# Kernel tuning notes

Hardware: AMD Instinct MI355X
Metric: run time of the kernel (lower is better)

The kernel has to match this reference:

```python
import jax, jax.numpy as jnp
import numpy as np

B, N, L, D, DI = 128, 64, 33, 512, 768  # batch, num_images, cooccurrence_num+1, CLIP dim, inst dim


def setup_inputs() -> dict:
    key = jax.random.key(0)
    ks = jax.random.split(key, 8)
    return {
        "image_features": jax.random.normal(ks[0], (B, N, D), jnp.float32),
        "image_mask": jax.random.randint(ks[1], (B, N), 0, 2).astype(jnp.int32),
        "landmark_feature": jax.random.normal(ks[2], (B, L, D), jnp.float32),
        "inst": jax.random.normal(ks[3], (B, DI), jnp.float32),
        # scoring_module = Linear(512+768 -> 512) -> ReLU -> LayerNorm(512) -> Dropout(eval: identity)
        "W_score": jax.random.normal(ks[4], (DI + D, D), jnp.float32) * 0.02,
        "b_score": jnp.zeros((D,), jnp.float32),
        "ln_gamma": jnp.ones((D,), jnp.float32),
        "ln_beta": jnp.zeros((D,), jnp.float32),
    }


def _l2norm(x):
    return x / jnp.linalg.norm(x, axis=-1, keepdims=True)


def reference(image_features, image_mask, landmark_feature, inst,
              W_score, b_score, ln_gamma, ln_beta):
    LN_EPS = 1e-12
    mask = image_mask == 1  # [B, N]

    img = _l2norm(image_features)          # [B, N, D]
    lmk = _l2norm(landmark_feature)        # [B, L, D]
    img = jnp.where(mask[:, :, None], img, 0.0)
    img_mean = img.mean(axis=1)            # [B, D]

    # scoring_module on cat([inst, img_mean]) -> ReLU -> LayerNorm (Dropout is identity in eval)
    h = jnp.concatenate([inst, img_mean], axis=-1) @ W_score + b_score  # [B, D]
    h = jax.nn.relu(h)
    mu = h.mean(axis=-1, keepdims=True)
    var = h.var(axis=-1, keepdims=True)    # biased, as in torch LayerNorm
    h = (h - mu) / jnp.sqrt(var + LN_EPS) * ln_gamma + ln_beta
    inst_feat = _l2norm(h)                 # [B, D]

    cooccurrence_weight = 100.0 * jnp.einsum('bd,bld->bl', inst_feat, lmk)  # [B, L]
    candidate_prob = 100.0 * jnp.einsum('bnd,bld->bnl', img, lmk)           # [B, N, L]
    candidate_prob = jnp.where(mask[:, :, None], candidate_prob, -jnp.inf)
    p = jax.nn.softmax(candidate_prob, axis=1)                              # softmax over images

    corrected_landmark_feature = jnp.einsum('bnl,bl,bld->bnd', p, cooccurrence_weight, lmk)  # [B, N, D]
    corrected_candidate_prob = jnp.einsum('bnl,bl->bn', p, cooccurrence_weight)              # [B, N]
    corrected_candidate_prob = jnp.where(mask, corrected_candidate_prob, -jnp.inf)
    return corrected_landmark_feature, corrected_candidate_prob
```

## Files before the change

kernel.cpp:

```cpp
#include <hip/hip_runtime.h>
#include <math.h>

#define BB 128
#define NN 64
#define LL 33
#define DD 512
#define DIN 768

#define NEG_BIG (-3.0e38f)

typedef __attribute__((ext_vector_type(8))) short bf16x8;
typedef __attribute__((ext_vector_type(4))) float f32x4;

#define WS_ASW   0
#define WS_BSW   (WS_ASW + BB*3*16*64*4)
#define WS_LMK16 (WS_BSW + BB*4*16*64*4)
#define WS_MEANP (WS_LMK16 + BB*LL*DD/2)
#define WS_PART  (WS_MEANP + BB*16*DD)
#define WS_INSTF (WS_PART + BB*8*DD)
#define WS_S     (WS_INSTF + BB*DD)

__device__ __forceinline__ float wave_sum(float v) {
#pragma unroll
  for (int m = 32; m; m >>= 1) v += __shfl_xor(v, m);
  return v;
}
__device__ __forceinline__ float wave_max(float v) {
#pragma unroll
  for (int m = 32; m; m >>= 1) v = fmaxf(v, __shfl_xor(v, m));
  return v;
}
__device__ __forceinline__ unsigned f2bf(float f) {
  unsigned u = __float_as_uint(f);
  return (u + 0x7FFFu + ((u >> 16) & 1u)) >> 16;
}
__device__ __forceinline__ unsigned pk2(float a, float b) {
  return f2bf(a) | (f2bf(b) << 16);
}
__device__ __forceinline__ float bflo(unsigned u) { return __uint_as_float(u << 16); }
__device__ __forceinline__ float bfhi(unsigned u) { return __uint_as_float(u & 0xFFFF0000u); }

__global__ __launch_bounds__(256) void k_prep_v15(
    const float* __restrict__ img_in, const int* __restrict__ mask,
    const float* __restrict__ lmk_in, unsigned int* __restrict__ AswW,
    unsigned int* __restrict__ BswW, unsigned short* __restrict__ lmk16,
    float* __restrict__ meanp) {
  uint4* Asw = (uint4*)AswW;
  uint4* Bsw = (uint4*)BswW;
  int o = blockIdx.x;
  int blk = (o & 7) * 64 + (o >> 3);
  int b = blk >> 2, q = blk & 3;
  int t = threadIdx.x;
  int w = t >> 6, lane = t & 63;

  int nbase = q * 16 + w * 4;
  const float4* ib = (const float4*)(img_in + ((size_t)b * NN + nbase) * DD);
  float4 r[4][2];
#pragma unroll
  for (int i = 0; i < 4; i++) {
    r[i][0] = ib[i * 128 + lane * 2];
    r[i][1] = ib[i * 128 + lane * 2 + 1];
  }
  const int* mb = mask + b * NN + nbase;
  float macc[8];
#pragma unroll
  for (int j = 0; j < 8; j++) macc[j] = 0.f;
#pragma unroll
  for (int i = 0; i < 4; i++) {
    float4 v0 = r[i][0], v1 = r[i][1];
    float ss = v0.x * v0.x + v0.y * v0.y + v0.z * v0.z + v0.w * v0.w +
               v1.x * v1.x + v1.y * v1.y + v1.z * v1.z + v1.w * v1.w;
    ss = wave_sum(ss);
    float keep = (mb[i] == 1) ? 1.f : 0.f;
    float s = keep / sqrtf(ss);
    v0.x *= s; v0.y *= s; v0.z *= s; v0.w *= s;
    v1.x *= s; v1.y *= s; v1.z *= s; v1.w *= s;
    macc[0] += v0.x; macc[1] += v0.y; macc[2] += v0.z; macc[3] += v0.w;
    macc[4] += v1.x; macc[5] += v1.y; macc[6] += v1.z; macc[7] += v1.w;
    int rg = nbase + i;
    uint4 p = make_uint4(pk2(v0.x, v0.y), pk2(v0.z, v0.w), pk2(v1.x, v1.y),
                         pk2(v1.z, v1.w));
    Bsw[(((size_t)b * 4 + (rg >> 4)) * 16 + (lane >> 2)) * 64 + (rg & 15) +
        16 * (lane & 3)] = p;
  }
  {
    float* mp = meanp + ((size_t)b * 16 + q * 4 + w) * DD + lane * 8;
    float4 m0 = {macc[0], macc[1], macc[2], macc[3]};
    float4 m1 = {macc[4], macc[5], macc[6], macc[7]};
    *(float4*)mp = m0;
    *(float4*)(mp + 4) = m1;
  }

  int lr = q * 8 + w * 2;
  bool xtra = (q == 0) && (w == 3);
  if (xtra) {
#pragma unroll
    for (int kk = 0; kk < 16; kk++)
      if (lane & 15)
        Asw[(((size_t)b * 3 + 2) * 16 + kk) * 64 + lane] = make_uint4(0, 0, 0, 0);
  }
#pragma unroll
  for (int k = 0; k < 3; k++) {
    int row = (k < 2) ? (lr + k) : 32;
    if (k == 2 && !xtra) break;
    const float4* lb = (const float4*)(lmk_in + ((size_t)b * LL + row) * DD);
    float4 v0 = lb[lane * 2], v1 = lb[lane * 2 + 1];
    float ss = v0.x * v0.x + v0.y * v0.y + v0.z * v0.z + v0.w * v0.w +
               v1.x * v1.x + v1.y * v1.y + v1.z * v1.z + v1.w * v1.w;
    ss = wave_sum(ss);
    float s = 1.f / sqrtf(ss);
    v0.x *= s; v0.y *= s; v0.z *= s; v0.w *= s;
    v1.x *= s; v1.y *= s; v1.z *= s; v1.w *= s;
    uint4 p = make_uint4(pk2(v0.x, v0.y), pk2(v0.z, v0.w), pk2(v1.x, v1.y),
                         pk2(v1.z, v1.w));
    ((uint4*)lmk16)[((size_t)b * LL + row) * 64 + lane] = p;
    Asw[(((size_t)b * 3 + (row >> 4)) * 16 + (lane >> 2)) * 64 + (row & 15) +
        16 * (lane & 3)] = p;
  }
}

#define KCH 160
__global__ void k_gemm_part_v15(const float* __restrict__ inst,
                                const float* __restrict__ meanp,
                                const float* __restrict__ W,
                                float* __restrict__ part) {
  int o = blockIdx.x;
  int blk = (o & 7) * 32 + (o >> 3);
  __shared__ float xs[KCH][4];
  int bg = blk >> 3;
  int c = blk & 7;
  int b0 = bg * 4;
  int t = threadIdx.x;
  int k0 = c * KCH;
  for (int i = t; i < KCH * 4; i += 256) {
    int kk = i >> 2;
    int j = i & 3;
    int kg = k0 + kk;
    float val;
    if (kg < DIN) {
      val = inst[(size_t)(b0 + j) * DIN + kg];
    } else {
      const float* mp = meanp + (size_t)(b0 + j) * 16 * DD + (kg - DIN);
      float s = 0.f;
#pragma unroll
      for (int p = 0; p < 16; p++) s += mp[p * DD];
      val = s * (1.f / 64.f);
    }
    xs[kk][j] = val;
  }
  __syncthreads();
  const float2* Wp = (const float2*)(W + (size_t)k0 * DD);
  float2 a0 = {0.f, 0.f}, a1 = {0.f, 0.f}, a2 = {0.f, 0.f}, a3 = {0.f, 0.f};
#pragma unroll 4
  for (int kk = 0; kk < KCH; kk++) {
    float2 w = Wp[kk * 256 + t];
    float4 xv = *(const float4*)&xs[kk][0];
    a0.x += xv.x * w.x; a0.y += xv.x * w.y;
    a1.x += xv.y * w.x; a1.y += xv.y * w.y;
    a2.x += xv.z * w.x; a2.y += xv.z * w.y;
    a3.x += xv.w * w.x; a3.y += xv.w * w.y;
  }
  float2* pp = (float2*)part;
  pp[(((size_t)(b0 + 0) * 8 + c) * DD >> 1) + t] = a0;
  pp[(((size_t)(b0 + 1) * 8 + c) * DD >> 1) + t] = a1;
  pp[(((size_t)(b0 + 2) * 8 + c) * DD >> 1) + t] = a2;
  pp[(((size_t)(b0 + 3) * 8 + c) * DD >> 1) + t] = a3;
}

__device__ __forceinline__ float blk_sum2(float v, float* red4, int t) {
  v = wave_sum(v);
  __syncthreads();
  if ((t & 63) == 0) red4[t >> 6] = v;
  __syncthreads();
  return red4[0] + red4[1] + red4[2] + red4[3];
}

__global__ __launch_bounds__(256) void k_ssm_v15(
    const unsigned int* __restrict__ AswW, const unsigned int* __restrict__ BswW,
    const float* __restrict__ part, const float* __restrict__ bias,
    const float* __restrict__ gamma, const float* __restrict__ beta,
    const unsigned short* __restrict__ lmk16, const int* __restrict__ mask,
    float* __restrict__ q) {
  __shared__ float st[16][68];
  __shared__ float fi[DD];
  __shared__ float red4[4];
  const bf16x8* Asw = (const bf16x8*)AswW;
  const bf16x8* Bsw = (const bf16x8*)BswW;
  int o = blockIdx.x;
  int blk = (o & 7) * 48 + (o >> 3);
  int b = blk / 3, mt = blk - b * 3;
  int t = threadIdx.x;
  int nt = t >> 6, lane = t & 63;

  {
    const float* pb = part + (size_t)b * 8 * DD;
    float sa = 0.f, sb = 0.f;
#pragma unroll
    for (int c = 0; c < 8; c++) {
      sa += pb[c * DD + t];
      sb += pb[c * DD + t + 256];
    }
    float rva = fmaxf(sa + bias[t], 0.f);
    float rvb = fmaxf(sb + bias[t + 256], 0.f);
    float s1 = blk_sum2(rva + rvb, red4, t);
    float s2 = blk_sum2(rva * rva + rvb * rvb, red4, t);
    float mu = s1 * (1.f / DD);
    float var = s2 * (1.f / DD) - mu * mu;
    float inv = 1.f / sqrtf(var + 1e-12f);
    float ya = (rva - mu) * inv * gamma[t] + beta[t];
    float yb = (rvb - mu) * inv * gamma[t + 256] + beta[t + 256];
    float n2 = blk_sum2(ya * ya + yb * yb, red4, t);
    float rn = 1.f / sqrtf(n2);
    fi[t] = ya * rn;
    fi[t + 256] = yb * rn;
  }

  {
    const bf16x8* ap = Asw + ((size_t)(b * 3 + mt) * 16) * 64 + lane;
    const bf16x8* bp = Bsw + ((size_t)(b * 4 + nt) * 16) * 64 + lane;
    f32x4 acc = {0.f, 0.f, 0.f, 0.f};
#pragma unroll
    for (int kk = 0; kk < 16; kk++)
      acc = __builtin_amdgcn_mfma_f32_16x16x32_bf16(ap[kk * 64], bp[kk * 64],
                                                    acc, 0, 0, 0);
    int col = nt * 16 + (lane & 15);
    int rbase = (lane >> 4) << 2;
#pragma unroll
    for (int reg = 0; reg < 4; reg++) st[rbase + reg][col] = 100.f * acc[reg];
  }
  __syncthreads();

  bool keep = (mask[b * NN + lane] == 1);
  const float4* fi4 = (const float4*)fi;
  float4 f0 = fi4[lane * 2], f1 = fi4[lane * 2 + 1];
#pragma unroll
  for (int j = 0; j < 4; j++) {
    int lrow = nt * 4 + j;
    int l = mt * 16 + lrow;
    if (l >= LL) break;
    float s = st[lrow][lane];
    uint4 u = ((const uint4*)(lmk16 + ((size_t)b * LL + l) * DD))[lane];
    float dp = f0.x * bflo(u.x) + f0.y * bfhi(u.x) + f0.z * bflo(u.y) +
               f0.w * bfhi(u.y) + f1.x * bflo(u.z) + f1.y * bfhi(u.z) +
               f1.z * bflo(u.w) + f1.w * bfhi(u.w);
    dp = wave_sum(dp);
    float cw = 100.f * dp;
    float v = keep ? s : NEG_BIG;
    float mx = wave_max(v);
    float e = keep ? __expf(s - mx) : 0.f;
    float Z = wave_sum(e);
    float sc = (Z > 0.f) ? (cw / Z) : 0.f;
    q[((size_t)b * LL + l) * NN + lane] = e * sc;
  }
}

__global__ void k_out_v15(const float* __restrict__ S,
                          const unsigned short* __restrict__ lmk16,
                          const int* __restrict__ mask,
                          float* __restrict__ out1,
                          float* __restrict__ out2) {
  __shared__ __align__(16) float qs[LL][8];
  int o = blockIdx.x;
  int blk = (o & 7) * 128 + (o >> 3);
  int b = blk >> 3;
  int nt = blk & 7;
  int t = threadIdx.x;
  for (int i = t; i < 8 * LL; i += 256) {
    int l = i >> 3;
    int n_loc = i & 7;
    qs[l][n_loc] = S[((size_t)b * LL + l) * NN + nt * 8 + n_loc];
  }
  __syncthreads();
  if (t < 8) {
    float ssum = 0.f;
#pragma unroll
    for (int l = 0; l < LL; l++) ssum += qs[l][t];
    int n = nt * 8 + t;
    out2[b * NN + n] = (mask[b * NN + n] == 1) ? ssum : NEG_BIG;
  }
  int d0 = t * 2;
  float accx[8], accy[8];
#pragma unroll
  for (int n = 0; n < 8; n++) { accx[n] = 0.f; accy[n] = 0.f; }
  const unsigned short* lmkb = lmk16 + (size_t)b * LL * DD;
#pragma unroll 4
  for (int l = 0; l < LL; l++) {
    unsigned u = *(const unsigned*)(lmkb + (size_t)l * DD + d0);
    float lvx = bflo(u), lvy = bfhi(u);
    float4 q0 = *(const float4*)&qs[l][0];
    float4 q1 = *(const float4*)&qs[l][4];
    accx[0] += q0.x * lvx; accy[0] += q0.x * lvy;
    accx[1] += q0.y * lvx; accy[1] += q0.y * lvy;
    accx[2] += q0.z * lvx; accy[2] += q0.z * lvy;
    accx[3] += q0.w * lvx; accy[3] += q0.w * lvy;
    accx[4] += q1.x * lvx; accy[4] += q1.x * lvy;
    accx[5] += q1.y * lvx; accy[5] += q1.y * lvy;
    accx[6] += q1.z * lvx; accy[6] += q1.z * lvy;
    accx[7] += q1.w * lvx; accy[7] += q1.w * lvy;
  }
#pragma unroll
  for (int n = 0; n < 8; n++) {
    float2 oo = {accx[n], accy[n]};
    *(float2*)&out1[(((size_t)b * NN) + nt * 8 + n) * DD + d0] = oo;
  }
}

extern "C" void kernel_launch(void* const* d_in, const int* in_sizes, int n_in,
                              void* d_out, int out_size, void* d_ws, size_t ws_size,
                              hipStream_t stream) {
  const float* image_features = (const float*)d_in[0];
  const int* image_mask = (const int*)d_in[1];
  const float* landmark = (const float*)d_in[2];
  const float* inst = (const float*)d_in[3];
  const float* W = (const float*)d_in[4];
  const float* bias = (const float*)d_in[5];
  const float* gamma = (const float*)d_in[6];
  const float* beta = (const float*)d_in[7];

  float* ws = (float*)d_ws;
  unsigned int* Asw = (unsigned int*)(ws + WS_ASW);
  unsigned int* Bsw = (unsigned int*)(ws + WS_BSW);
  unsigned short* lmk16 = (unsigned short*)(ws + WS_LMK16);
  float* ws_meanp = ws + WS_MEANP;
  float* ws_part = ws + WS_PART;
  float* ws_S = ws + WS_S;

  float* out1 = (float*)d_out;
  float* out2 = (float*)d_out + (size_t)BB * NN * DD;

  k_prep_v15<<<BB * 4, 256, 0, stream>>>(image_features, image_mask, landmark,
                                         Asw, Bsw, lmk16, ws_meanp);
  k_gemm_part_v15<<<(BB / 4) * 8, 256, 0, stream>>>(inst, ws_meanp, W, ws_part);
  k_ssm_v15<<<BB * 3, 256, 0, stream>>>((const unsigned int*)Asw,
                                        (const unsigned int*)Bsw, ws_part, bias,
                                        gamma, beta, lmk16, image_mask, ws_S);
  k_out_v15<<<BB * 8, 256, 0, stream>>>(ws_S, lmk16, image_mask, out1, out2);
}
```

Measured before the change: 48.96 us.

## Overlap inst-part GEMM with prep kernel and pre-reduce image mean in-block

Splits the scoring GEMM into two parts. The inst half (K=768) runs as extra blocks inside the prep kernel, so it overlaps with the normalization work. The image-mean half runs in a small follow-up kernel. The prep blocks now reduce their four waves' partial means through shared memory before writing, which cuts the meanp partials from 16 to 4 per batch. This lowers the work left on the critical path after prep, at the cost of a heterogeneous prep launch and 16 partials per batch to sum in the ssm kernel.

```diff
diff --git a/kernel.cpp b/kernel.cpp
--- a/kernel.cpp
+++ b/kernel.cpp
@@ -16,9 +16,8 @@
 #define WS_BSW   (WS_ASW + BB*3*16*64*4)
 #define WS_LMK16 (WS_BSW + BB*4*16*64*4)
 #define WS_MEANP (WS_LMK16 + BB*LL*DD/2)
-#define WS_PART  (WS_MEANP + BB*16*DD)
-#define WS_INSTF (WS_PART + BB*8*DD)
-#define WS_S     (WS_INSTF + BB*DD)
+#define WS_PART  (WS_MEANP + BB*4*DD)
+#define WS_S     (WS_PART + BB*16*DD)
 
 __device__ __forceinline__ float wave_sum(float v) {
 #pragma unroll
@@ -40,119 +39,148 @@
 __device__ __forceinline__ float bflo(unsigned u) { return __uint_as_float(u << 16); }
 __device__ __forceinline__ float bfhi(unsigned u) { return __uint_as_float(u & 0xFFFF0000u); }
 
-__global__ __launch_bounds__(256) void k_prep_v15(
+__global__ __launch_bounds__(256) void k_prep_v16(
     const float* __restrict__ img_in, const int* __restrict__ mask,
-    const float* __restrict__ lmk_in, unsigned int* __restrict__ AswW,
+    const float* __restrict__ lmk_in, const float* __restrict__ inst,
+    const float* __restrict__ W, unsigned int* __restrict__ AswW,
     unsigned int* __restrict__ BswW, unsigned short* __restrict__ lmk16,
-    float* __restrict__ meanp) {
-  uint4* Asw = (uint4*)AswW;
-  uint4* Bsw = (uint4*)BswW;
+    float* __restrict__ meanp, float* __restrict__ part) {
+  __shared__ __align__(16) float shbuf[2048];
+  int t = threadIdx.x;
+
+  if (blockIdx.x < 512) {
+    uint4* Asw = (uint4*)AswW;
+    uint4* Bsw = (uint4*)BswW;
+    int o = blockIdx.x;
+    int blk = (o & 7) * 64 + (o >> 3);
+    int b = blk >> 2, q = blk & 3;
+    int w = t >> 6, lane = t & 63;
+
+    int nbase = q * 16 + w * 4;
+    const float4* ib = (const float4*)(img_in + ((size_t)b * NN + nbase) * DD);
+    float4 r[4][2];
+#pragma unroll
+    for (int i = 0; i < 4; i++) {
+      r[i][0] = ib[i * 128 + lane * 2];
+      r[i][1] = ib[i * 128 + lane * 2 + 1];
+    }
+    const int* mb = mask + b * NN + nbase;
+    float macc[8];
+#pragma unroll
+    for (int j = 0; j < 8; j++) macc[j] = 0.f;
+#pragma unroll
+    for (int i = 0; i < 4; i++) {
+      float4 v0 = r[i][0], v1 = r[i][1];
+      float ss = v0.x * v0.x + v0.y * v0.y + v0.z * v0.z + v0.w * v0.w +
+                 v1.x * v1.x + v1.y * v1.y + v1.z * v1.z + v1.w * v1.w;
+      ss = wave_sum(ss);
+      float keep = (mb[i] == 1) ? 1.f : 0.f;
+      float s = keep / sqrtf(ss);
+      v0.x *= s; v0.y *= s; v0.z *= s; v0.w *= s;
+      v1.x *= s; v1.y *= s; v1.z *= s; v1.w *= s;
+      macc[0] += v0.x; macc[1] += v0.y; macc[2] += v0.z; macc[3] += v0.w;
+      macc[4] += v1.x; macc[5] += v1.y; macc[6] += v1.z; macc[7] += v1.w;
+      int rg = nbase + i;
+      uint4 p = make_uint4(pk2(v0.x, v0.y), pk2(v0.z, v0.w), pk2(v1.x, v1.y),
+                           pk2(v1.z, v1.w));
+      Bsw[(((size_t)b * 4 + (rg >> 4)) * 16 + (lane >> 2)) * 64 + (rg & 15) +
+          16 * (lane & 3)] = p;
+    }
+    {
+      float4 m0 = {macc[0], macc[1], macc[2], macc[3]};
+      float4 m1 = {macc[4], macc[5], macc[6], macc[7]};
+      *(float4*)&shbuf[w * 512 + lane * 8] = m0;
+      *(float4*)&shbuf[w * 512 + lane * 8 + 4] = m1;
+    }
+    __syncthreads();
+    {
+      float s0 = shbuf[t] + shbuf[512 + t] + shbuf[1024 + t] + shbuf[1536 + t];
+      float s1 = shbuf[t + 256] + shbuf[512 + t + 256] + shbuf[1024 + t + 256] +
+                 shbuf[1536 + t + 256];
+      meanp[((size_t)b * 4 + q) * DD + t] = s0;
+      meanp[((size_t)b * 4 + q) * DD + t + 256] = s1;
+    }
+
+    int lr = q * 8 + w * 2;
+    bool xtra = (q == 0) && (w == 3);
+    if (xtra) {
+#pragma unroll
+      for (int kk = 0; kk < 16; kk++)
+        if (lane & 15)
+          Asw[(((size_t)b * 3 + 2) * 16 + kk) * 64 + lane] =
+              make_uint4(0, 0, 0, 0);
+    }
+#pragma unroll
+    for (int k = 0; k < 3; k++) {
+      int row = (k < 2) ? (lr + k) : 32;
+      if (k == 2 && !xtra) break;
+      const float4* lb = (const float4*)(lmk_in + ((size_t)b * LL + row) * DD);
+      float4 v0 = lb[lane * 2], v1 = lb[lane * 2 + 1];
+      float ss = v0.x * v0.x + v0.y * v0.y + v0.z * v0.z + v0.w * v0.w +
+                 v1.x * v1.x + v1.y * v1.y + v1.z * v1.z + v1.w * v1.w;
+      ss = wave_sum(ss);
+      float s = 1.f / sqrtf(ss);
+      v0.x *= s; v0.y *= s; v0.z *= s; v0.w *= s;
+      v1.x *= s; v1.y *= s; v1.z *= s; v1.w *= s;
+      uint4 p = make_uint4(pk2(v0.x, v0.y), pk2(v0.z, v0.w), pk2(v1.x, v1.y),
+                           pk2(v1.z, v1.w));
+      ((uint4*)lmk16)[((size_t)b * LL + row) * 64 + lane] = p;
+      Asw[(((size_t)b * 3 + (row >> 4)) * 16 + (lane >> 2)) * 64 + (row & 15) +
+          16 * (lane & 3)] = p;
+    }
+  } else {
+    float(*xs)[4] = (float(*)[4])shbuf;
+    int g = blockIdx.x - 512;
+    int gs = (g & 7) * 32 + (g >> 3);
+    int bg = gs >> 3, c = gs & 7;
+    int b0 = bg * 4;
+    int k0 = c * 96;
+    for (int i = t; i < 96 * 4; i += 256) {
+      int kk = i >> 2;
+      int j = i & 3;
+      xs[kk][j] = inst[(size_t)(b0 + j) * DIN + k0 + kk];
+    }
+    __syncthreads();
+    const float2* Wp = (const float2*)(W + (size_t)k0 * DD);
+    float2 a0 = {0.f, 0.f}, a1 = {0.f, 0.f}, a2 = {0.f, 0.f}, a3 = {0.f, 0.f};
+#pragma unroll 4
+    for (int kk = 0; kk < 96; kk++) {
+      float2 w = Wp[kk * 256 + t];
+      float4 xv = *(const float4*)&xs[kk][0];
+      a0.x += xv.x * w.x; a0.y += xv.x * w.y;
+      a1.x += xv.y * w.x; a1.y += xv.y * w.y;
+      a2.x += xv.z * w.x; a2.y += xv.z * w.y;
+      a3.x += xv.w * w.x; a3.y += xv.w * w.y;
+    }
+    float2* pp = (float2*)part;
+    pp[(((size_t)(b0 + 0) * 16 + c) * DD >> 1) + t] = a0;
+    pp[(((size_t)(b0 + 1) * 16 + c) * DD >> 1) + t] = a1;
+    pp[(((size_t)(b0 + 2) * 16 + c) * DD >> 1) + t] = a2;
+    pp[(((size_t)(b0 + 3) * 16 + c) * DD >> 1) + t] = a3;
+  }
+}
+
+__global__ __launch_bounds__(256) void k_gbot_v16(
+    const float* __restrict__ meanp, const float* __restrict__ W,
+    float* __restrict__ part) {
+  __shared__ float xs[64][4];
   int o = blockIdx.x;
-  int blk = (o & 7) * 64 + (o >> 3);
-  int b = blk >> 2, q = blk & 3;
-  int t = threadIdx.x;
-  int w = t >> 6, lane = t & 63;
-
-  int nbase = q * 16 + w * 4;
-  const float4* ib = (const float4*)(img_in + ((size_t)b * NN + nbase) * DD);
-  float4 r[4][2];
-#pragma unroll
-  for (int i = 0; i < 4; i++) {
-    r[i][0] = ib[i * 128 + lane * 2];
-    r[i][1] = ib[i * 128 + lane * 2 + 1];
-  }
-  const int* mb = mask + b * NN + nbase;
-  float macc[8];
-#pragma unroll
-  for (int j = 0; j < 8; j++) macc[j] = 0.f;
-#pragma unroll
-  for (int i = 0; i < 4; i++) {
-    float4 v0 = r[i][0], v1 = r[i][1];
-    float ss = v0.x * v0.x + v0.y * v0.y + v0.z * v0.z + v0.w * v0.w +
-               v1.x * v1.x + v1.y * v1.y + v1.z * v1.z + v1.w * v1.w;
-    ss = wave_sum(ss);
-    float keep = (mb[i] == 1) ? 1.f : 0.f;
-    float s = keep / sqrtf(ss);
-    v0.x *= s; v0.y *= s; v0.z *= s; v0.w *= s;
-    v1.x *= s; v1.y *= s; v1.z *= s; v1.w *= s;
-    macc[0] += v0.x; macc[1] += v0.y; macc[2] += v0.z; macc[3] += v0.w;
-    macc[4] += v1.x; macc[5] += v1.y; macc[6] += v1.z; macc[7] += v1.w;
-    int rg = nbase + i;
-    uint4 p = make_uint4(pk2(v0.x, v0.y), pk2(v0.z, v0.w), pk2(v1.x, v1.y),
-                         pk2(v1.z, v1.w));
-    Bsw[(((size_t)b * 4 + (rg >> 4)) * 16 + (lane >> 2)) * 64 + (rg & 15) +
-        16 * (lane & 3)] = p;
-  }
-  {
-    float* mp = meanp + ((size_t)b * 16 + q * 4 + w) * DD + lane * 8;
-    float4 m0 = {macc[0], macc[1], macc[2], macc[3]};
-    float4 m1 = {macc[4], macc[5], macc[6], macc[7]};
-    *(float4*)mp = m0;
-    *(float4*)(mp + 4) = m1;
-  }
-
-  int lr = q * 8 + w * 2;
-  bool xtra = (q == 0) && (w == 3);
-  if (xtra) {
-#pragma unroll
-    for (int kk = 0; kk < 16; kk++)
-      if (lane & 15)
-        Asw[(((size_t)b * 3 + 2) * 16 + kk) * 64 + lane] = make_uint4(0, 0, 0, 0);
-  }
-#pragma unroll
-  for (int k = 0; k < 3; k++) {
-    int row = (k < 2) ? (lr + k) : 32;
-    if (k == 2 && !xtra) break;
-    const float4* lb = (const float4*)(lmk_in + ((size_t)b * LL + row) * DD);
-    float4 v0 = lb[lane * 2], v1 = lb[lane * 2 + 1];
-    float ss = v0.x * v0.x + v0.y * v0.y + v0.z * v0.z + v0.w * v0.w +
-               v1.x * v1.x + v1.y * v1.y + v1.z * v1.z + v1.w * v1.w;
-    ss = wave_sum(ss);
-    float s = 1.f / sqrtf(ss);
-    v0.x *= s; v0.y *= s; v0.z *= s; v0.w *= s;
-    v1.x *= s; v1.y *= s; v1.z *= s; v1.w *= s;
-    uint4 p = make_uint4(pk2(v0.x, v0.y), pk2(v0.z, v0.w), pk2(v1.x, v1.y),
-                         pk2(v1.z, v1.w));
-    ((uint4*)lmk16)[((size_t)b * LL + row) * 64 + lane] = p;
-    Asw[(((size_t)b * 3 + (row >> 4)) * 16 + (lane >> 2)) * 64 + (row & 15) +
-        16 * (lane & 3)] = p;
-  }
-}
-
-#define KCH 160
-__global__ void k_gemm_part_v15(const float* __restrict__ inst,
-                                const float* __restrict__ meanp,
-                                const float* __restrict__ W,
-                                float* __restrict__ part) {
-  int o = blockIdx.x;
-  int blk = (o & 7) * 32 + (o >> 3);
-  __shared__ float xs[KCH][4];
-  int bg = blk >> 3;
-  int c = blk & 7;
+  int gs = (o & 7) * 32 + (o >> 3);
+  int bg = gs >> 3, c = gs & 7;
   int b0 = bg * 4;
   int t = threadIdx.x;
-  int k0 = c * KCH;
-  for (int i = t; i < KCH * 4; i += 256) {
-    int kk = i >> 2;
-    int j = i & 3;
-    int kg = k0 + kk;
-    float val;
-    if (kg < DIN) {
-      val = inst[(size_t)(b0 + j) * DIN + kg];
-    } else {
-      const float* mp = meanp + (size_t)(b0 + j) * 16 * DD + (kg - DIN);
-      float s = 0.f;
-#pragma unroll
-      for (int p = 0; p < 16; p++) s += mp[p * DD];
-      val = s * (1.f / 64.f);
-    }
-    xs[kk][j] = val;
-  }
-  __syncthreads();
-  const float2* Wp = (const float2*)(W + (size_t)k0 * DD);
+  int kloc0 = c * 64;
+  if (t < 64 * 4) {
+    int kk = t >> 2;
+    int j = t & 3;
+    const float* mp = meanp + (size_t)(b0 + j) * 4 * DD + kloc0 + kk;
+    xs[kk][j] = (mp[0] + mp[DD] + mp[2 * DD] + mp[3 * DD]) * (1.f / 64.f);
+  }
+  __syncthreads();
+  const float2* Wp = (const float2*)(W + (size_t)(DIN + kloc0) * DD);
   float2 a0 = {0.f, 0.f}, a1 = {0.f, 0.f}, a2 = {0.f, 0.f}, a3 = {0.f, 0.f};
 #pragma unroll 4
-  for (int kk = 0; kk < KCH; kk++) {
+  for (int kk = 0; kk < 64; kk++) {
     float2 w = Wp[kk * 256 + t];
     float4 xv = *(const float4*)&xs[kk][0];
     a0.x += xv.x * w.x; a0.y += xv.x * w.y;
@@ -161,10 +189,10 @@
     a3.x += xv.w * w.x; a3.y += xv.w * w.y;
   }
   float2* pp = (float2*)part;
-  pp[(((size_t)(b0 + 0) * 8 + c) * DD >> 1) + t] = a0;
-  pp[(((size_t)(b0 + 1) * 8 + c) * DD >> 1) + t] = a1;
-  pp[(((size_t)(b0 + 2) * 8 + c) * DD >> 1) + t] = a2;
-  pp[(((size_t)(b0 + 3) * 8 + c) * DD >> 1) + t] = a3;
+  pp[(((size_t)(b0 + 0) * 16 + 8 + c) * DD >> 1) + t] = a0;
+  pp[(((size_t)(b0 + 1) * 16 + 8 + c) * DD >> 1) + t] = a1;
+  pp[(((size_t)(b0 + 2) * 16 + 8 + c) * DD >> 1) + t] = a2;
+  pp[(((size_t)(b0 + 3) * 16 + 8 + c) * DD >> 1) + t] = a3;
 }
 
 __device__ __forceinline__ float blk_sum2(float v, float* red4, int t) {
@@ -175,7 +203,7 @@
   return red4[0] + red4[1] + red4[2] + red4[3];
 }
 
-__global__ __launch_bounds__(256) void k_ssm_v15(
+__global__ __launch_bounds__(256) void k_ssm_v16(
     const unsigned int* __restrict__ AswW, const unsigned int* __restrict__ BswW,
     const float* __restrict__ part, const float* __restrict__ bias,
     const float* __restrict__ gamma, const float* __restrict__ beta,
@@ -193,10 +221,10 @@
   int nt = t >> 6, lane = t & 63;
 
   {
-    const float* pb = part + (size_t)b * 8 * DD;
+    const float* pb = part + (size_t)b * 16 * DD;
     float sa = 0.f, sb = 0.f;
 #pragma unroll
-    for (int c = 0; c < 8; c++) {
+    for (int c = 0; c < 16; c++) {
       sa += pb[c * DD + t];
       sb += pb[c * DD + t + 256];
     }
@@ -254,7 +282,7 @@
   }
 }
 
-__global__ void k_out_v15(const float* __restrict__ S,
+__global__ void k_out_v16(const float* __restrict__ S,
                           const unsigned short* __restrict__ lmk16,
                           const int* __restrict__ mask,
                           float* __restrict__ out1,
@@ -328,11 +356,12 @@
   float* out1 = (float*)d_out;
   float* out2 = (float*)d_out + (size_t)BB * NN * DD;
 
-  k_prep_v15<<<BB * 4, 256, 0, stream>>>(image_features, image_mask, landmark,
-                                         Asw, Bsw, lmk16, ws_meanp);
-  k_gemm_part_v15<<<(BB / 4) * 8, 256, 0, stream>>>(inst, ws_meanp, W, ws_part);
-  k_ssm_v15<<<BB * 3, 256, 0, stream>>>((const unsigned int*)Asw,
+  k_prep_v16<<<768, 256, 0, stream>>>(image_features, image_mask, landmark,
+                                      inst, W, Asw, Bsw, lmk16, ws_meanp,
+                                      ws_part);
+  k_gbot_v16<<<256, 256, 0, stream>>>(ws_meanp, W, ws_part);
+  k_ssm_v16<<<BB * 3, 256, 0, stream>>>((const unsigned int*)Asw,
                                         (const unsigned int*)Bsw, ws_part, bias,
                                         gamma, beta, lmk16, image_mask, ws_S);
-  k_out_v15<<<BB * 8, 256, 0, stream>>>(ws_S, lmk16, image_mask, out1, out2);
-}
+  k_out_v16<<<BB * 8, 256, 0, stream>>>(ws_S, lmk16, image_mask, out1, out2);
+}
```

After: 45.53 us. 7.0% less time.
